# Kernel tuning notes

Hardware: AMD Instinct MI355X
Metric: run time of the kernel (lower is better)

## Reference

```python
import jax, jax.numpy as jnp
import numpy as np

KS = 3          # kernel_size
PAD = 1         # padding
N = KS * KS     # 9 sampling points
S2 = 2 ** 0.5
ANGLES = [0, 45, 90, 135, 180]

# angle-dependent extra offsets (x, y), indexed by angle // 45
_OFF = {
    0: ([0.0] * 9, [0.0] * 9),
    1: ([1 - S2, 1 - S2 * 0.5, 1, -S2 * 0.5, 0, S2 * 0.5, -1, S2 * 0.5 - 1, S2 - 1],
        [1, S2 * 0.5, S2 - 1, 1 - S2 * 0.5, 0, S2 * 0.5 - 1, 1 - S2, -S2 * 0.5, -1]),
    2: ([0, 1, 2, -1, 0, 1, -2, -1, 0],
        [2, 1, 0, 1, 0, -1, 0, -1, -2]),
    3: ([1, 1 + S2 * 0.5, 1 + S2, -S2 * 0.5, 0, S2 * 0.5, -1 - S2, -1 - S2 * 0.5, -1],
        [1 + S2, S2 * 0.5, -1, 1 + S2 * 0.5, 0, -1 - S2 * 0.5, 1, -S2 * 0.5, 1 + S2]),
    4: ([2, 2, 2, 0, 0, 0, -2, -2, -2],
        [2, 0, -2, 2, 0, -2, 2, 0, -2]),
}


def _deform_sample(x, angle):
    """Bilinear gather of the rotated 3x3 sampling grid -> (b,c,h*KS,w*KS)."""
    b, c, h, w = x.shape
    xp = jnp.pad(x, ((0, 0), (0, 0), (PAD, PAD), (PAD, PAD)))  # zero padding
    ph, pw = h + 2 * PAD, w + 2 * PAD

    ox_l, oy_l = _OFF[angle // 45]
    ox = jnp.asarray(np.array(ox_l, dtype=np.float32))
    oy = jnp.asarray(np.array(oy_l, dtype=np.float32))

    rng = np.arange(-(KS - 1) // 2, (KS - 1) // 2 + 1)
    pnx_np, pny_np = np.meshgrid(rng, rng, indexing='ij')  # torch default 'ij'
    pnx = jnp.asarray(pnx_np.reshape(-1).astype(np.float32))
    pny = jnp.asarray(pny_np.reshape(-1).astype(np.float32))

    # p = p_0 + p_n + offset ; keep x as (h,1,N) and y as (1,w,N), broadcast later
    px = jnp.arange(1, h + 1, dtype=jnp.float32)[:, None, None] + (pnx + ox)[None, None, :]  # (h,1,N)
    py = jnp.arange(1, w + 1, dtype=jnp.float32)[None, :, None] + (pny + oy)[None, None, :]  # (1,w,N)

    fx, fy = jnp.floor(px), jnp.floor(py)
    ql_x = jnp.clip(fx, 0, ph - 1)       # left-top row
    qr_x = jnp.clip(fx + 1, 0, ph - 1)   # right-bottom row
    ql_y = jnp.clip(fy, 0, pw - 1)
    qr_y = jnp.clip(fy + 1, 0, pw - 1)

    pxc = jnp.clip(px, 0, ph - 1)
    pyc = jnp.clip(py, 0, pw - 1)

    g_lt = (1 + (ql_x - pxc)) * (1 + (ql_y - pyc))  # (h,w,N) after broadcast
    g_rb = (1 - (qr_x - pxc)) * (1 - (qr_y - pyc))
    g_lb = (1 + (ql_x - pxc)) * (1 - (qr_y - pyc))
    g_rt = (1 - (qr_x - pxc)) * (1 + (ql_y - pyc))

    xf = xp.reshape(b, c, ph * pw)

    def gather(qx, qy):
        idx = qx.astype(jnp.int32) * pw + qy.astype(jnp.int32)      # (h,w,N)
        idx = jnp.broadcast_to(idx, (h, w, N)).reshape(-1)
        return jnp.take(xf, idx, axis=2).reshape(b, c, h, w, N)

    xo = (jnp.broadcast_to(g_lt, (h, w, N))[None, None] * gather(ql_x, ql_y)
          + jnp.broadcast_to(g_rb, (h, w, N))[None, None] * gather(qr_x, qr_y)
          + jnp.broadcast_to(g_lb, (h, w, N))[None, None] * gather(ql_x, qr_y)
          + jnp.broadcast_to(g_rt, (h, w, N))[None, None] * gather(qr_x, ql_y))

    # (b,c,h,w,N) -> (b,c,h*KS,w*KS) matching torch _reshape_x_offset
    xo = xo.reshape(b, c, h, w, KS, KS).transpose(0, 1, 2, 4, 3, 5).reshape(b, c, h * KS, w * KS)
    return xo


def _conv(xo, weight):
    # baseline_conv: stride=1, padding=0, no bias
    return jax.lax.conv_general_dilated(
        xo, weight, window_strides=(1, 1), padding='VALID',
        dimension_numbers=('NCHW', 'OIHW', 'NCHW'))


def setup_inputs() -> dict:
    key = jax.random.key(0)
    kx, kw = jax.random.split(key)
    x = jax.random.normal(kx, (2, 256, 64, 64), dtype=jnp.float32)
    weight = jax.random.normal(kw, (256, 256, 3, 3), dtype=jnp.float32) * 0.02
    return {"x": x, "weight": weight}


def reference(x, weight):
    return tuple(_conv(_deform_sample(x, a), weight) for a in ANGLES)
```

## Files before the change

kernel.cpp:

```cpp
#include <hip/hip_runtime.h>
#include <hip/hip_bf16.h>
#include <stdint.h>


#define S2F 1.41421356237309515f

__constant__ float c_ox[5][9] = {
  {0.f,0.f,0.f,0.f,0.f,0.f,0.f,0.f,0.f},
  {1.f-S2F, 1.f-S2F*0.5f, 1.f, -S2F*0.5f, 0.f, S2F*0.5f, -1.f, S2F*0.5f-1.f, S2F-1.f},
  {0.f,1.f,2.f,-1.f,0.f,1.f,-2.f,-1.f,0.f},
  {1.f, 1.f+S2F*0.5f, 1.f+S2F, -S2F*0.5f, 0.f, S2F*0.5f, -1.f-S2F, -1.f-S2F*0.5f, -1.f},
  {2.f,2.f,2.f,0.f,0.f,0.f,-2.f,-2.f,-2.f}
};
__constant__ float c_oy[5][9] = {
  {0.f,0.f,0.f,0.f,0.f,0.f,0.f,0.f,0.f},
  {1.f, S2F*0.5f, S2F-1.f, 1.f-S2F*0.5f, 0.f, S2F*0.5f-1.f, 1.f-S2F, -S2F*0.5f, -1.f},
  {2.f,1.f,0.f,1.f,0.f,-1.f,0.f,-1.f,-2.f},
  {1.f+S2F, S2F*0.5f, -1.f, 1.f+S2F*0.5f, 0.f, -1.f-S2F*0.5f, 1.f, -S2F*0.5f, 1.f+S2F},
  {2.f,0.f,-2.f,2.f,0.f,-2.f,2.f,0.f,-2.f}
};

typedef __bf16 bf16x8_t __attribute__((ext_vector_type(8)));
typedef float f32x4_t __attribute__((ext_vector_type(4)));

typedef const __attribute__((address_space(1))) void* as1cp;
typedef __attribute__((address_space(3))) void* as3p;

__device__ __forceinline__ void gload16(const void* g, void* l) {
  __builtin_amdgcn_global_load_lds((as1cp)g, (as3p)l, 16, 0, 0);
}

__global__ void k_transpose(const float* __restrict__ x, float* __restrict__ xT) {
  const int v = blockIdx.x, u = blockIdx.y, b = blockIdx.z;
  const int ic = threadIdx.x;
  xT[(((b*64 + u)*64 + v)*256) + ic] =
      x[(((b*256 + ic)*64 + u)*64) + v];
}

__global__ void k_wconv(const float* __restrict__ w, __hip_bfloat16* __restrict__ wb) {
  const int tid = blockIdx.x*256 + threadIdx.x;
  const int t = tid >> 16;
  const int rem = tid & 65535;
  const int oc = rem >> 8;
  const int ic = rem & 255;
  wb[tid] = __float2bfloat16(w[(oc*256 + ic)*9 + t]);
}

__global__ void k_sample(const float* __restrict__ xT,
                         __hip_bfloat16* __restrict__ xo, int a0)
{
  const int aidx = a0 + blockIdx.z;
  __hip_bfloat16* xoa = xo + (size_t)blockIdx.z * (2ull*192*192*256);

  const int tid = threadIdx.x;
  const int ic = (tid & 63) * 4;
  const int j = blockIdx.x*4 + (tid >> 6);
  const int i = blockIdx.y;

  const int a = i / 3, r = i - 3*a;
  const int bc = j / 3, s = j - 3*bc;
  const int n = r*3 + s;
  const float px = (float)(a + r) + c_ox[aidx][n];
  const float py = (float)(bc + s) + c_oy[aidx][n];
  const float fx = floorf(px), fy = floorf(py);
  const float pxc = fminf(fmaxf(px, 0.f), 65.f);
  const float pyc = fminf(fmaxf(py, 0.f), 65.f);
  const int qlx = (int)fminf(fmaxf(fx,      0.f), 65.f);
  const int qrx = (int)fminf(fmaxf(fx + 1.f, 0.f), 65.f);
  const int qly = (int)fminf(fmaxf(fy,      0.f), 65.f);
  const int qry = (int)fminf(fmaxf(fy + 1.f, 0.f), 65.f);

  const bool inxl = (qlx >= 1) && (qlx <= 64);
  const bool inyl = (qly >= 1) && (qly <= 64);

  const size_t o0 = (((size_t)0*192 + i)*192 + j)*256 + ic;
  const size_t o1 = (((size_t)1*192 + i)*192 + j)*256 + ic;
  const f32x4_t zero = (f32x4_t){0.f,0.f,0.f,0.f};

  if (px == fx && py == fy) {
    #pragma unroll
    for (int b = 0; b < 2; ++b) {
      const float* xb = xT + (size_t)b * (64*64*256);
      f32x4_t v = (inxl && inyl) ? *(const f32x4_t*)&xb[((qlx-1)*64 + (qly-1))*256 + ic] : zero;
      ushort4 pk;
      pk.x = __hip_bfloat16_raw(__float2bfloat16(v[0])).x;
      pk.y = __hip_bfloat16_raw(__float2bfloat16(v[1])).x;
      pk.z = __hip_bfloat16_raw(__float2bfloat16(v[2])).x;
      pk.w = __hip_bfloat16_raw(__float2bfloat16(v[3])).x;
      *(ushort4*)&xoa[b ? o1 : o0] = pk;
    }
    return;
  }

  const float wlx = 1.f + (float)qlx - pxc;
  const float wrx = 1.f - (float)qrx + pxc;
  const float wly = 1.f + (float)qly - pyc;
  const float wry = 1.f - (float)qry + pyc;
  const float glt = wlx*wly, grb = wrx*wry, glb = wlx*wry, grt = wrx*wly;

  const bool inxr = (qrx >= 1) && (qrx <= 64);
  const bool inyr = (qry >= 1) && (qry <= 64);

  #pragma unroll
  for (int b = 0; b < 2; ++b) {
    const float* xb = xT + (size_t)b * (64*64*256);
    f32x4_t vlt = (inxl && inyl) ? *(const f32x4_t*)&xb[((qlx-1)*64 + (qly-1))*256 + ic] : zero;
    f32x4_t vrb = (inxr && inyr) ? *(const f32x4_t*)&xb[((qrx-1)*64 + (qry-1))*256 + ic] : zero;
    f32x4_t vlb = (inxl && inyr) ? *(const f32x4_t*)&xb[((qlx-1)*64 + (qry-1))*256 + ic] : zero;
    f32x4_t vrt = (inxr && inyl) ? *(const f32x4_t*)&xb[((qrx-1)*64 + (qly-1))*256 + ic] : zero;
    ushort4 pk;
    float v0 = glt*vlt[0] + grb*vrb[0] + glb*vlb[0] + grt*vrt[0];
    float v1 = glt*vlt[1] + grb*vrb[1] + glb*vlb[1] + grt*vrt[1];
    float v2 = glt*vlt[2] + grb*vrb[2] + glb*vlb[2] + grt*vrt[2];
    float v3 = glt*vlt[3] + grb*vrb[3] + glb*vlb[3] + grt*vrt[3];
    pk.x = __hip_bfloat16_raw(__float2bfloat16(v0)).x;
    pk.y = __hip_bfloat16_raw(__float2bfloat16(v1)).x;
    pk.z = __hip_bfloat16_raw(__float2bfloat16(v2)).x;
    pk.w = __hip_bfloat16_raw(__float2bfloat16(v3)).x;
    *(ushort4*)&xoa[b ? o1 : o0] = pk;
  }
}

__global__ __launch_bounds__(256, 2) void k_conv(
    const __hip_bfloat16* __restrict__ xo,
    const __hip_bfloat16* __restrict__ wb,
    float* __restrict__ out)
{
  __shared__ __align__(16) char smem[66048];
  const int tid = threadIdx.x;

  const int f = blockIdx.x;
  const int T = gridDim.x & ~15;
  int pairI, nt;
  if (f < T) { pairI = (f >> 4)*8 + (f & 7); nt = (f >> 3) & 1; }
  else       { pairI = (T >> 1) + ((f - T) >> 1); nt = f & 1; }
  const int ct = pairI % 3;
  const int yz = pairI / 3;
  const int i0 = (yz % 95) * 2;
  const int z  = yz / 95;
  const int oc0 = nt * 128;
  const int j0 = ct * 64;

  const int q8   = tid >> 3;
  const int slot = tid & 7;
  const int wv   = tid >> 6;
  const int sw   = slot ^ (q8 & 7);

  const char* xob = (const char*)xo + (size_t)z * 18874368u;
  const char* wbc = (const char*)wb;

  int arow[4], acol[4], brow[4];
  #pragma unroll
  for (int p = 0; p < 4; ++p) {
    const int m = p*32 + q8;
    arow[p] = i0 + (m >> 6);
    acol[p] = j0 + (m & 63);
    brow[p] = oc0 + m;
  }

  f32x4_t acc[4][4];
  #pragma unroll
  for (int fm = 0; fm < 4; ++fm)
    #pragma unroll
    for (int fn = 0; fn < 4; ++fn)
      acc[fm][fn] = (f32x4_t){0.f, 0.f, 0.f, 0.f};

  const int lane = tid & 63;
  const int lrow = lane & 15;
  const int lk   = lane >> 4;
  const int wm   = wv >> 1;
  const int wn   = wv & 1;

  auto stage = [&](int kk, int cur) {
    const int icg = kk / 9;
    const int t   = kk - icg*9;
    const int ki = t / 3, kj = t - 3*ki;
    char* sa = smem + cur*16384 + wv*1024;
    char* sb = smem + 32768 + cur*16384 + wv*1024;
    #pragma unroll
    for (int p = 0; p < 4; ++p) {
      int col = acol[p] + kj; col = (col > 191) ? 191 : col;
      const char* ga = xob + (((arow[p] + ki)*192 + col)*256 + icg*64)*2 + sw*16;
      gload16(ga, sa + p*4096);
      const char* gb = wbc + ((t*256 + brow[p])*256 + icg*64)*2 + sw*16;
      gload16(gb, sb + p*4096);
    }
  };

  auto compute = [&](int cur) {
    const char* sa = smem + cur*16384;
    const char* sb = smem + 32768 + cur*16384;
    bf16x8_t af[4][2], bfr[4][2];
    #pragma unroll
    for (int fi = 0; fi < 4; ++fi) {
      const int m = wm*64 + fi*16 + lrow;
      const int n = wn*64 + fi*16 + lrow;
      #pragma unroll
      for (int ks = 0; ks < 2; ++ks) {
        af[fi][ks]  = *(const bf16x8_t*)(sa + m*128 + (((ks*4 + lk) ^ (m & 7)) * 16));
        bfr[fi][ks] = *(const bf16x8_t*)(sb + n*128 + (((ks*4 + lk) ^ (n & 7)) * 16));
      }
    }
    #pragma unroll
    for (int fm = 0; fm < 4; ++fm)
      #pragma unroll
      for (int fn = 0; fn < 4; ++fn)
        #pragma unroll
        for (int ks = 0; ks < 2; ++ks)
          acc[fm][fn] = __builtin_amdgcn_mfma_f32_16x16x32_bf16(
              af[fm][ks], bfr[fn][ks], acc[fm][fn], 0, 0, 0);
  };

  stage(0, 0);
  __syncthreads();
  for (int kk = 0; kk < 36; ++kk) {
    const int cur = kk & 1;
    if (kk < 35) stage(kk + 1, cur ^ 1);
    compute(cur);
    __syncthreads();
  }

  float* eps = (float*)smem;
  #pragma unroll
  for (int fm = 0; fm < 4; ++fm)
    #pragma unroll
    for (int fn = 0; fn < 4; ++fn)
      #pragma unroll
      for (int r = 0; r < 4; ++r)
        eps[(wn*64 + fn*16 + lrow)*129 + (wm*64 + fm*16 + lk*4 + r)] = acc[fm][fn][r];
  __syncthreads();

  float* outb = out + (size_t)z * 9241600u;
  #pragma unroll
  for (int pass = 0; pass < 16; ++pass) {
    const int ocw = pass*8 + (tid >> 5);
    const int m4  = (tid & 31) * 4;
    const int di  = m4 >> 6, jc = m4 & 63;
    const int i = i0 + di, j = j0 + jc;
    const float v0 = eps[ocw*129 + m4 + 0];
    const float v1 = eps[ocw*129 + m4 + 1];
    const float v2 = eps[ocw*129 + m4 + 2];
    const float v3 = eps[ocw*129 + m4 + 3];
    float* dst = outb + ((size_t)(oc0 + ocw)*190 + i)*190 + j;
    if (j + 3 < 190) {
      *(float2*)dst       = make_float2(v0, v1);
      *(float2*)(dst + 2) = make_float2(v2, v3);
    } else {
      if (j     < 190) dst[0] = v0;
      if (j + 1 < 190) dst[1] = v1;
      if (j + 2 < 190) dst[2] = v2;
      if (j + 3 < 190) dst[3] = v3;
    }
  }
}

extern "C" void kernel_launch(void* const* d_in, const int* in_sizes, int n_in,
                              void* d_out, int out_size, void* d_ws, size_t ws_size,
                              hipStream_t stream)
{
  const float* x = (const float*)d_in[0];
  const float* w = (const float*)d_in[1];
  float* out = (float*)d_out;

  char* ws = (char*)d_ws;
  float*          xT = (float*)ws;
  __hip_bfloat16* wb = (__hip_bfloat16*)(ws + 8388608);
  __hip_bfloat16* xo = (__hip_bfloat16*)(ws + 9568256);

  const bool merged = (ws_size >= 198311936ull);

  k_transpose<<<dim3(64, 64, 2), 256, 0, stream>>>(x, xT);
  k_wconv<<<2304, 256, 0, stream>>>(w, wb);

  if (merged) {
    k_sample<<<dim3(48, 192, 5), 256, 0, stream>>>(xT, xo, 0);
    k_conv<<<5700, 256, 0, stream>>>(xo, wb, out);
  } else {
    for (int aidx = 0; aidx < 5; ++aidx) {
      k_sample<<<dim3(48, 192, 1), 256, 0, stream>>>(xT, xo, aidx);
      k_conv<<<1140, 256, 0, stream>>>(xo, wb, out + (size_t)aidx * 18483200u);
    }
  }
}
```

Measured before the change: 524.1 us.

## Triple-buffer A tiles with explicit vmcnt waits in conv GEMM pipeline

Restructures the conv kernel's main loop so activation tiles are prefetched two steps ahead in a three-slot LDS ring, while weight tiles stay double-buffered. Block-wide __syncthreads is replaced by partial s_waitcnt vmcnt plus s_barrier, so the next step's loads stay in flight during compute. LDS moves to dynamic allocation of 80 KB per block, up from about 64.5 KB. With launch_bounds(256,2) that is 160 KB for two blocks per CU, which could limit occupancy if the LDS budget is smaller.

```diff
diff --git a/kernel.cpp b/kernel.cpp
--- a/kernel.cpp
+++ b/kernel.cpp
@@ -126,7 +126,7 @@
     const __hip_bfloat16* __restrict__ wb,
     float* __restrict__ out)
 {
-  __shared__ __align__(16) char smem[66048];
+  extern __shared__ __align__(16) char smem[];
   const int tid = threadIdx.x;
 
   const int f = blockIdx.x;
@@ -171,25 +171,32 @@
   const int wm   = wv >> 1;
   const int wn   = wv & 1;
 
-  auto stage = [&](int kk, int cur) {
+  auto stageA = [&](int kk, int s) {
     const int icg = kk / 9;
     const int t   = kk - icg*9;
     const int ki = t / 3, kj = t - 3*ki;
-    char* sa = smem + cur*16384 + wv*1024;
-    char* sb = smem + 32768 + cur*16384 + wv*1024;
+    char* sa = smem + s*16384 + wv*1024;
     #pragma unroll
     for (int p = 0; p < 4; ++p) {
       int col = acol[p] + kj; col = (col > 191) ? 191 : col;
       const char* ga = xob + (((arow[p] + ki)*192 + col)*256 + icg*64)*2 + sw*16;
       gload16(ga, sa + p*4096);
+    }
+  };
+  auto stageB = [&](int kk, int b) {
+    const int icg = kk / 9;
+    const int t   = kk - icg*9;
+    char* sb = smem + 49152 + b*16384 + wv*1024;
+    #pragma unroll
+    for (int p = 0; p < 4; ++p) {
       const char* gb = wbc + ((t*256 + brow[p])*256 + icg*64)*2 + sw*16;
       gload16(gb, sb + p*4096);
     }
   };
 
-  auto compute = [&](int cur) {
-    const char* sa = smem + cur*16384;
-    const char* sb = smem + 32768 + cur*16384;
+  auto compute = [&](int s, int b) {
+    const char* sa = smem + s*16384;
+    const char* sb = smem + 49152 + b*16384;
     bf16x8_t af[4][2], bfr[4][2];
     #pragma unroll
     for (int fi = 0; fi < 4; ++fi) {
@@ -211,15 +218,26 @@
               af[fm][ks], bfr[fn][ks], acc[fm][fn], 0, 0, 0);
   };
 
-  stage(0, 0);
+  stageA(0, 0);
+  stageB(0, 0);
+  stageA(1, 1);
+  asm volatile("s_waitcnt vmcnt(4)" ::: "memory");
+  __builtin_amdgcn_s_barrier();
+
+  int cs = 0, ss = 2;
+  for (int kk = 0; kk < 36; ++kk) {
+    if (kk < 35) stageB(kk + 1, (kk + 1) & 1);
+    if (kk < 34) stageA(kk + 2, ss);
+    compute(cs, kk & 1);
+    if (kk < 34)       { asm volatile("s_waitcnt vmcnt(4)" ::: "memory");
+                         __builtin_amdgcn_s_barrier(); }
+    else if (kk == 34) { asm volatile("s_waitcnt vmcnt(0)" ::: "memory");
+                         __builtin_amdgcn_s_barrier(); }
+    cs = (cs == 2) ? 0 : cs + 1;
+    ss = (ss == 2) ? 0 : ss + 1;
+  }
+
   __syncthreads();
-  for (int kk = 0; kk < 36; ++kk) {
-    const int cur = kk & 1;
-    if (kk < 35) stage(kk + 1, cur ^ 1);
-    compute(cur);
-    __syncthreads();
-  }
-
   float* eps = (float*)smem;
   #pragma unroll
   for (int fm = 0; fm < 4; ++fm)
@@ -269,16 +287,19 @@
 
   const bool merged = (ws_size >= 198311936ull);
 
+  (void)hipFuncSetAttribute((const void*)k_conv,
+                            hipFuncAttributeMaxDynamicSharedMemorySize, 81920);
+
   k_transpose<<<dim3(64, 64, 2), 256, 0, stream>>>(x, xT);
   k_wconv<<<2304, 256, 0, stream>>>(w, wb);
 
   if (merged) {
     k_sample<<<dim3(48, 192, 5), 256, 0, stream>>>(xT, xo, 0);
-    k_conv<<<5700, 256, 0, stream>>>(xo, wb, out);
+    k_conv<<<5700, 256, 81920, stream>>>(xo, wb, out);
   } else {
     for (int aidx = 0; aidx < 5; ++aidx) {
       k_sample<<<dim3(48, 192, 1), 256, 0, stream>>>(xT, xo, aidx);
-      k_conv<<<1140, 256, 0, stream>>>(xo, wb, out + (size_t)aidx * 18483200u);
-    }
-  }
-}
+      k_conv<<<1140, 256, 81920, stream>>>(xo, wb, out + (size_t)aidx * 18483200u);
+    }
+  }
+}
```

Result: faster. 510.8 us (median of 3 runs) (-2.5%).
